# Performance work log

Measured on AMD Instinct MI355X. Metric: run time of the kernel, lower is better.

## Reference

```python
import jax, jax.numpy as jnp
import numpy as np

WIN = 7
K1, K2 = 0.01, 0.03


def _box_filter(x, w):
    """Valid-padding uniform box filter. x: (B, D, H, W); w: (1, 1, k, k)."""
    B, D, H, Wd = x.shape
    k = w.shape[-1]
    y = jax.lax.conv_general_dilated(
        x.reshape(B * D, 1, H, Wd), w, window_strides=(1, 1), padding='VALID',
        dimension_numbers=('NCHW', 'OIHW', 'NCHW'))
    return y.reshape(B, D, H - k + 1, Wd - k + 1)


def setup_inputs() -> dict:
    key = jax.random.key(0)
    kx, ky = jax.random.split(key)
    X = jax.random.uniform(kx, (4, 64, 256, 256), dtype=jnp.float32)
    Y = jax.random.uniform(ky, (4, 64, 256, 256), dtype=jnp.float32)
    w = jnp.ones((1, 1, WIN, WIN), dtype=jnp.float32) / (WIN * WIN)  # buffer self.w
    return {"X": X, "Y": Y, "w": w}


def reference(X, Y, w):
    data_range = 1.0
    C1 = (K1 * data_range) ** 2
    C2 = (K2 * data_range) ** 2
    NP = WIN * WIN
    cov_norm = NP / (NP - 1)

    ux = _box_filter(X, w)
    uy = _box_filter(Y, w)
    uxx = _box_filter(X * X, w)
    uyy = _box_filter(Y * Y, w)
    uxy = _box_filter(X * Y, w)

    vx = cov_norm * (uxx - ux * ux)
    vy = cov_norm * (uyy - uy * uy)
    vxy = cov_norm * (uxy - ux * uy)

    A1 = 2.0 * ux * uy + C1
    A2 = 2.0 * vxy + C2
    B1 = ux * ux + uy * uy + C1
    B2 = vx + vy + C2
    S = (A1 * A2) / (B1 * B2)  # (B, D, H', W')

    # Faithful to torch: ssim_per_slice[:, i] = S_i.mean() (mean over batch AND spatial),
    # then 1 - mean over depth, returned per batch element.
    slice_means = S.mean(axis=(0, 2, 3))  # (D,)
    loss = 1.0 - slice_means.mean()
    return jnp.full((X.shape[0],), loss, dtype=X.dtype)
```

## Files before the change

### kernel.cpp

```cpp
#include <hip/hip_runtime.h>

#define H 256
#define W 256
#define W4 (W / 4)
#define OWID 250
#define NIMG 256
#define BAND 10
#define NBANDS 25
#define NBLK (NBANDS * NIMG)
#define RIN 16
#define WPB 4
#define NBLOCKS (NBLK / WPB)


__device__ __forceinline__ float4 f4zero() { return make_float4(0.f, 0.f, 0.f, 0.f); }

#define CC1 1e-4f
#define CC2 9e-4f
#define KAA (1.f / 2401.f)
#define K2A (2.f / 2401.f)
#define KT1 (1.f / 24.f)
#define KT2 (-1.f / 1176.f)
#define KT3 (1.f / 48.f)
#define KT4 (-1.f / 2352.f)

struct Ctx {
    const float4* Xp;
    const float4* Yp;
    float4 sx, sy, sxy, spp;
    float4 ex[3], ey[3];
    float4 lx, ly;
};

__device__ __forceinline__ void hwin4(const float4 S, float w[4]) {
    const float p1 = S.x;
    const float p2 = p1 + S.y;
    const float p3 = p2 + S.z;
    const float E  = p3 + S.w;
    const float n3 = __shfl_down(p3, 1);
    const float nE = __shfl_down(E, 1);
    const float f1 = __shfl_down(p1, 2);
    const float f2 = __shfl_down(p2, 2);
    w[0] = E + n3;
    w[1] = (E - p1) + nE;
    w[2] = (E - p2) + nE + f1;
    w[3] = (E - p3) + nE + f2;
}

template<int R>
__device__ __forceinline__ void step(Ctx& c, const float m01, const float m23,
                                     float& lsum) {
    const float4 xn = c.ex[R % 3], yn = c.ey[R % 3];
    float4 xo = f4zero(), yo = f4zero();
    if constexpr (R >= 7) { xo = c.lx; yo = c.ly; }

    if constexpr (R + 3 < RIN) {
        c.ex[R % 3] = c.Xp[(R + 3) * W4];
        c.ey[R % 3] = c.Yp[(R + 3) * W4];
    }
    if constexpr (R >= 6 && R <= 14) {
        c.lx = c.Xp[(R - 6) * W4];
        c.ly = c.Yp[(R - 6) * W4];
    }

    c.sx.x += xn.x - xo.x; c.sx.y += xn.y - xo.y;
    c.sx.z += xn.z - xo.z; c.sx.w += xn.w - xo.w;
    c.sy.x += yn.x - yo.x; c.sy.y += yn.y - yo.y;
    c.sy.z += yn.z - yo.z; c.sy.w += yn.w - yo.w;
    c.sxy.x = fmaf(xn.x, yn.x, fmaf(-xo.x, yo.x, c.sxy.x));
    c.sxy.y = fmaf(xn.y, yn.y, fmaf(-xo.y, yo.y, c.sxy.y));
    c.sxy.z = fmaf(xn.z, yn.z, fmaf(-xo.z, yo.z, c.sxy.z));
    c.sxy.w = fmaf(xn.w, yn.w, fmaf(-xo.w, yo.w, c.sxy.w));
    c.spp.x = fmaf(xn.x, xn.x, fmaf(yn.x, yn.x, fmaf(-xo.x, xo.x, fmaf(-yo.x, yo.x, c.spp.x))));
    c.spp.y = fmaf(xn.y, xn.y, fmaf(yn.y, yn.y, fmaf(-xo.y, xo.y, fmaf(-yo.y, yo.y, c.spp.y))));
    c.spp.z = fmaf(xn.z, xn.z, fmaf(yn.z, yn.z, fmaf(-xo.z, xo.z, fmaf(-yo.z, yo.z, c.spp.z))));
    c.spp.w = fmaf(xn.w, xn.w, fmaf(yn.w, yn.w, fmaf(-xo.w, xo.w, fmaf(-yo.w, yo.w, c.spp.w))));

    if constexpr (R >= 6) {
        float wx[4], wy[4], wpp[4], wxy[4];
        hwin4(c.sx,  wx);
        hwin4(c.sy,  wy);
        hwin4(c.spp, wpp);
        hwin4(c.sxy, wxy);
        #pragma unroll
        for (int s = 0; s < 4; ++s) {
            const float P  = wx[s] * wy[s];
            const float Qs = fmaf(wy[s], wy[s], wx[s] * wx[s]);
            const float A1 = fmaf(K2A, P, CC1);
            const float B1 = fmaf(KAA, Qs, CC1);
            const float A2 = fmaf(KT1, wxy[s], fmaf(KT2, P, CC2));
            const float B2 = fmaf(KT3, wpp[s], fmaf(KT4, Qs, CC2));
            const float S  = (A1 * A2) * __builtin_amdgcn_rcpf(B1 * B2);
            lsum = fmaf(S, (s < 2) ? m01 : m23, lsum);
        }
    }
    if constexpr (R + 1 < RIN) step<R + 1>(c, m01, m23, lsum);
}

__global__ __launch_bounds__(256) void ssim_band_kernel(
    const float* __restrict__ X, const float* __restrict__ Y,
    float* __restrict__ partial)
{
    const int lane = threadIdx.x & 63;
    const int wid  = blockIdx.x * WPB + (threadIdx.x >> 6);
    const int img  = wid / NBANDS;
    const int band = wid % NBANDS;
    const int r0 = band * BAND;

    Ctx c;
    c.Xp = (const float4*)X + ((size_t)img * H + r0) * W4 + lane;
    c.Yp = (const float4*)Y + ((size_t)img * H + r0) * W4 + lane;
    c.sx = f4zero(); c.sy = f4zero(); c.sxy = f4zero(); c.spp = f4zero();
    c.ex[0] = c.Xp[0];      c.ey[0] = c.Yp[0];
    c.ex[1] = c.Xp[W4];     c.ey[1] = c.Yp[W4];
    c.ex[2] = c.Xp[2 * W4]; c.ey[2] = c.Yp[2 * W4];
    c.lx = f4zero(); c.ly = f4zero();

    const float m01 = (lane <= 62) ? 1.0f : 0.0f;
    const float m23 = (lane <= 61) ? 1.0f : 0.0f;

    float lsum = 0.0f;
    step<0>(c, m01, m23, lsum);

    #pragma unroll
    for (int off = 32; off > 0; off >>= 1)
        lsum += __shfl_down(lsum, off, 64);
    if (lane == 0) partial[wid] = lsum;
}

__global__ __launch_bounds__(256) void ssim_reduce_kernel(
    const float* __restrict__ partial, float* __restrict__ out)
{
    const int tid = threadIdx.x;
    double acc = 0.0;
    for (int i = tid; i < NBLK; i += 256)
        acc += (double)partial[i];
    #pragma unroll
    for (int off = 32; off > 0; off >>= 1)
        acc += __shfl_down(acc, off, 64);
    __shared__ double wsumd[4];
    if ((tid & 63) == 0) wsumd[tid >> 6] = acc;
    __syncthreads();
    if (tid == 0) {
        double total = wsumd[0] + wsumd[1] + wsumd[2] + wsumd[3];
        float loss = (float)(1.0 - total / 16000000.0);
        out[0] = loss; out[1] = loss; out[2] = loss; out[3] = loss;
    }
}

extern "C" void kernel_launch(void* const* d_in, const int* in_sizes, int n_in,
                              void* d_out, int out_size, void* d_ws, size_t ws_size,
                              hipStream_t stream) {
    const float* X = (const float*)d_in[0];
    const float* Y = (const float*)d_in[1];
    float* out = (float*)d_out;
    float* partial = (float*)d_ws;

    hipLaunchKernelGGL(ssim_band_kernel, dim3(NBLOCKS), dim3(256), 0, stream,
                       X, Y, partial);
    hipLaunchKernelGGL(ssim_reduce_kernel, dim3(1), dim3(256), 0, stream,
                       partial, out);
}
```

Baseline: 158.8 us.

## Stage input rows into an LDS ring via direct global-to-LDS loads

Each wave now streams its band's rows of X and Y into a per-wave LDS ring buffer using global_load_lds with a prefetch distance of two rows. Rows leaving the vertical window are read back from LDS, so the second global reload of old rows goes away. The block size also drops from four waves to two. This trims global traffic and register pressure, but adds LDS use (about 20KB per wave), LDS reads and hand-written waitcnt synchronisation. The shallower prefetch depth may expose more memory latency.

```diff
diff --git a/kernel.cpp b/kernel.cpp
--- a/kernel.cpp
+++ b/kernel.cpp
@@ -9,8 +9,10 @@
 #define NBANDS 25
 #define NBLK (NBANDS * NIMG)
 #define RIN 16
-#define WPB 4
+#define WPB 2
 #define NBLOCKS (NBLK / WPB)
+#define NR 10
+#define PF 2
 
 
 __device__ __forceinline__ float4 f4zero() { return make_float4(0.f, 0.f, 0.f, 0.f); }
@@ -24,13 +26,18 @@
 #define KT3 (1.f / 48.f)
 #define KT4 (-1.f / 2352.f)
 
-struct Ctx {
-    const float4* Xp;
-    const float4* Yp;
-    float4 sx, sy, sxy, spp;
-    float4 ex[3], ey[3];
-    float4 lx, ly;
-};
+__device__ __forceinline__ void stage(const float4* g, float* l) {
+    __builtin_amdgcn_global_load_lds(
+        (const __attribute__((address_space(1))) unsigned int*)g,
+        (__attribute__((address_space(3))) unsigned int*)l,
+        16, 0, 0);
+}
+
+template<int N> __device__ __forceinline__ void wait_vm() {
+    if constexpr (N >= 4)      asm volatile("s_waitcnt vmcnt(4)" ::: "memory");
+    else if constexpr (N == 2) asm volatile("s_waitcnt vmcnt(2)" ::: "memory");
+    else                       asm volatile("s_waitcnt vmcnt(0)" ::: "memory");
+}
 
 __device__ __forceinline__ void hwin4(const float4 S, float w[4]) {
     const float p1 = S.x;
@@ -47,41 +54,54 @@
     w[3] = (E - p3) + nE + f2;
 }
 
+struct K {
+    const float4* Xp;
+    const float4* Yp;
+    float* rx;
+    float* ry;
+    float4 sx, sy, sxy, spp;
+    float m01, m23, lsum;
+    int lane;
+};
+
 template<int R>
-__device__ __forceinline__ void step(Ctx& c, const float m01, const float m23,
-                                     float& lsum) {
-    const float4 xn = c.ex[R % 3], yn = c.ey[R % 3];
+__device__ __forceinline__ void step(K& k) {
+    asm volatile("s_waitcnt lgkmcnt(0)" ::: "memory");
+
+    if constexpr (R + PF < RIN) {
+        stage(k.Xp + (R + PF) * W4, k.rx + ((R + PF) % NR) * W);
+        stage(k.Yp + (R + PF) * W4, k.ry + ((R + PF) % NR) * W);
+    }
+    constexpr int REM = RIN - 1 - R;
+    wait_vm<2 * (REM < PF ? REM : PF)>();
+
+    const float4 xn = *(const float4*)(k.rx + (R % NR) * W + k.lane * 4);
+    const float4 yn = *(const float4*)(k.ry + (R % NR) * W + k.lane * 4);
     float4 xo = f4zero(), yo = f4zero();
-    if constexpr (R >= 7) { xo = c.lx; yo = c.ly; }
-
-    if constexpr (R + 3 < RIN) {
-        c.ex[R % 3] = c.Xp[(R + 3) * W4];
-        c.ey[R % 3] = c.Yp[(R + 3) * W4];
-    }
-    if constexpr (R >= 6 && R <= 14) {
-        c.lx = c.Xp[(R - 6) * W4];
-        c.ly = c.Yp[(R - 6) * W4];
+    if constexpr (R >= 7) {
+        xo = *(const float4*)(k.rx + ((R - 7) % NR) * W + k.lane * 4);
+        yo = *(const float4*)(k.ry + ((R - 7) % NR) * W + k.lane * 4);
     }
 
-    c.sx.x += xn.x - xo.x; c.sx.y += xn.y - xo.y;
-    c.sx.z += xn.z - xo.z; c.sx.w += xn.w - xo.w;
-    c.sy.x += yn.x - yo.x; c.sy.y += yn.y - yo.y;
-    c.sy.z += yn.z - yo.z; c.sy.w += yn.w - yo.w;
-    c.sxy.x = fmaf(xn.x, yn.x, fmaf(-xo.x, yo.x, c.sxy.x));
-    c.sxy.y = fmaf(xn.y, yn.y, fmaf(-xo.y, yo.y, c.sxy.y));
-    c.sxy.z = fmaf(xn.z, yn.z, fmaf(-xo.z, yo.z, c.sxy.z));
-    c.sxy.w = fmaf(xn.w, yn.w, fmaf(-xo.w, yo.w, c.sxy.w));
-    c.spp.x = fmaf(xn.x, xn.x, fmaf(yn.x, yn.x, fmaf(-xo.x, xo.x, fmaf(-yo.x, yo.x, c.spp.x))));
-    c.spp.y = fmaf(xn.y, xn.y, fmaf(yn.y, yn.y, fmaf(-xo.y, xo.y, fmaf(-yo.y, yo.y, c.spp.y))));
-    c.spp.z = fmaf(xn.z, xn.z, fmaf(yn.z, yn.z, fmaf(-xo.z, xo.z, fmaf(-yo.z, yo.z, c.spp.z))));
-    c.spp.w = fmaf(xn.w, xn.w, fmaf(yn.w, yn.w, fmaf(-xo.w, xo.w, fmaf(-yo.w, yo.w, c.spp.w))));
+    k.sx.x += xn.x - xo.x; k.sx.y += xn.y - xo.y;
+    k.sx.z += xn.z - xo.z; k.sx.w += xn.w - xo.w;
+    k.sy.x += yn.x - yo.x; k.sy.y += yn.y - yo.y;
+    k.sy.z += yn.z - yo.z; k.sy.w += yn.w - yo.w;
+    k.sxy.x = fmaf(xn.x, yn.x, fmaf(-xo.x, yo.x, k.sxy.x));
+    k.sxy.y = fmaf(xn.y, yn.y, fmaf(-xo.y, yo.y, k.sxy.y));
+    k.sxy.z = fmaf(xn.z, yn.z, fmaf(-xo.z, yo.z, k.sxy.z));
+    k.sxy.w = fmaf(xn.w, yn.w, fmaf(-xo.w, yo.w, k.sxy.w));
+    k.spp.x = fmaf(xn.x, xn.x, fmaf(yn.x, yn.x, fmaf(-xo.x, xo.x, fmaf(-yo.x, yo.x, k.spp.x))));
+    k.spp.y = fmaf(xn.y, xn.y, fmaf(yn.y, yn.y, fmaf(-xo.y, xo.y, fmaf(-yo.y, yo.y, k.spp.y))));
+    k.spp.z = fmaf(xn.z, xn.z, fmaf(yn.z, yn.z, fmaf(-xo.z, xo.z, fmaf(-yo.z, yo.z, k.spp.z))));
+    k.spp.w = fmaf(xn.w, xn.w, fmaf(yn.w, yn.w, fmaf(-xo.w, xo.w, fmaf(-yo.w, yo.w, k.spp.w))));
 
     if constexpr (R >= 6) {
         float wx[4], wy[4], wpp[4], wxy[4];
-        hwin4(c.sx,  wx);
-        hwin4(c.sy,  wy);
-        hwin4(c.spp, wpp);
-        hwin4(c.sxy, wxy);
+        hwin4(k.sx,  wx);
+        hwin4(k.sy,  wy);
+        hwin4(k.spp, wpp);
+        hwin4(k.sxy, wxy);
         #pragma unroll
         for (int s = 0; s < 4; ++s) {
             const float P  = wx[s] * wy[s];
@@ -91,37 +111,44 @@
             const float A2 = fmaf(KT1, wxy[s], fmaf(KT2, P, CC2));
             const float B2 = fmaf(KT3, wpp[s], fmaf(KT4, Qs, CC2));
             const float S  = (A1 * A2) * __builtin_amdgcn_rcpf(B1 * B2);
-            lsum = fmaf(S, (s < 2) ? m01 : m23, lsum);
+            k.lsum = fmaf(S, (s < 2) ? k.m01 : k.m23, k.lsum);
         }
     }
-    if constexpr (R + 1 < RIN) step<R + 1>(c, m01, m23, lsum);
+    if constexpr (R + 1 < RIN) step<R + 1>(k);
 }
 
-__global__ __launch_bounds__(256) void ssim_band_kernel(
+__global__ __launch_bounds__(128) void ssim_band_kernel(
     const float* __restrict__ X, const float* __restrict__ Y,
     float* __restrict__ partial)
 {
-    const int lane = threadIdx.x & 63;
-    const int wid  = blockIdx.x * WPB + (threadIdx.x >> 6);
-    const int img  = wid / NBANDS;
-    const int band = wid % NBANDS;
+    __shared__ float ring[WPB][2][NR][W];
+
+    const int lane  = threadIdx.x & 63;
+    const int wslot = threadIdx.x >> 6;
+    const int wid   = blockIdx.x * WPB + wslot;
+    const int img   = wid / NBANDS;
+    const int band  = wid % NBANDS;
     const int r0 = band * BAND;
 
-    Ctx c;
-    c.Xp = (const float4*)X + ((size_t)img * H + r0) * W4 + lane;
-    c.Yp = (const float4*)Y + ((size_t)img * H + r0) * W4 + lane;
-    c.sx = f4zero(); c.sy = f4zero(); c.sxy = f4zero(); c.spp = f4zero();
-    c.ex[0] = c.Xp[0];      c.ey[0] = c.Yp[0];
-    c.ex[1] = c.Xp[W4];     c.ey[1] = c.Yp[W4];
-    c.ex[2] = c.Xp[2 * W4]; c.ey[2] = c.Yp[2 * W4];
-    c.lx = f4zero(); c.ly = f4zero();
+    K k;
+    k.Xp = (const float4*)X + ((size_t)img * H + r0) * W4 + lane;
+    k.Yp = (const float4*)Y + ((size_t)img * H + r0) * W4 + lane;
+    k.rx = &ring[wslot][0][0][0];
+    k.ry = &ring[wslot][1][0][0];
+    k.sx = f4zero(); k.sy = f4zero(); k.sxy = f4zero(); k.spp = f4zero();
+    k.lane = lane;
+    k.m01 = (lane <= 62) ? 1.0f : 0.0f;
+    k.m23 = (lane <= 61) ? 1.0f : 0.0f;
+    k.lsum = 0.0f;
 
-    const float m01 = (lane <= 62) ? 1.0f : 0.0f;
-    const float m23 = (lane <= 61) ? 1.0f : 0.0f;
+    stage(k.Xp,            k.rx);
+    stage(k.Yp,            k.ry);
+    stage(k.Xp + W4,       k.rx + W);
+    stage(k.Yp + W4,       k.ry + W);
 
-    float lsum = 0.0f;
-    step<0>(c, m01, m23, lsum);
+    step<0>(k);
 
+    float lsum = k.lsum;
     #pragma unroll
     for (int off = 32; off > 0; off >>= 1)
         lsum += __shfl_down(lsum, off, 64);
@@ -156,7 +183,7 @@
     float* out = (float*)d_out;
     float* partial = (float*)d_ws;
 
-    hipLaunchKernelGGL(ssim_band_kernel, dim3(NBLOCKS), dim3(256), 0, stream,
+    hipLaunchKernelGGL(ssim_band_kernel, dim3(NBLOCKS), dim3(128), 0, stream,
                        X, Y, partial);
     hipLaunchKernelGGL(ssim_reduce_kernel, dim3(1), dim3(256), 0, stream,
                        partial, out);
```

New measurement: 179.3 us. 12.9% more time.

## Process two images per wave and reload evicted rows instead of caching

Applied to the files above, without the earlier changes.

Each wave now handles the same band in two images (img and img+128), interleaving two independent sliding-window chains to raise instruction-level parallelism while halving the wave count to 3200. The lookahead buffers shrink to one row and the rows leaving the window are re-read from memory (expected cache hits) rather than held in registers. The goal is better latency hiding per wave. The cost is fewer waves in flight and more load instructions, which could hurt occupancy-based latency hiding.

```diff
diff --git a/kernel.cpp b/kernel.cpp
--- a/kernel.cpp
+++ b/kernel.cpp
@@ -2,15 +2,14 @@
 
 #define H 256
 #define W 256
-#define W4 (W / 4)
 #define OWID 250
-#define NIMG 256
 #define BAND 10
 #define NBANDS 25
-#define NBLK (NBANDS * NIMG)
+#define NW 3200
+#define WPB 4
+#define NBLOCKS (NW / WPB)
 #define RIN 16
-#define WPB 4
-#define NBLOCKS (NBLK / WPB)
+#define ROWB 1024
 
 
 __device__ __forceinline__ float4 f4zero() { return make_float4(0.f, 0.f, 0.f, 0.f); }
@@ -24,13 +23,27 @@
 #define KT3 (1.f / 48.f)
 #define KT4 (-1.f / 2352.f)
 
-struct Ctx {
-    const float4* Xp;
-    const float4* Yp;
-    float4 sx, sy, sxy, spp;
-    float4 ex[3], ey[3];
-    float4 lx, ly;
-};
+struct M4 { float4 sx, sy, sxy, spp; };
+
+__device__ __forceinline__ float4 ld16(const char* b, int off) {
+    return *(const float4*)(b + off);
+}
+
+__device__ __forceinline__ void slide(M4& m, const float4 xn, const float4 yn,
+                                      const float4 xo, const float4 yo) {
+    m.sx.x += xn.x - xo.x; m.sx.y += xn.y - xo.y;
+    m.sx.z += xn.z - xo.z; m.sx.w += xn.w - xo.w;
+    m.sy.x += yn.x - yo.x; m.sy.y += yn.y - yo.y;
+    m.sy.z += yn.z - yo.z; m.sy.w += yn.w - yo.w;
+    m.sxy.x = fmaf(xn.x, yn.x, fmaf(-xo.x, yo.x, m.sxy.x));
+    m.sxy.y = fmaf(xn.y, yn.y, fmaf(-xo.y, yo.y, m.sxy.y));
+    m.sxy.z = fmaf(xn.z, yn.z, fmaf(-xo.z, yo.z, m.sxy.z));
+    m.sxy.w = fmaf(xn.w, yn.w, fmaf(-xo.w, yo.w, m.sxy.w));
+    m.spp.x = fmaf(xn.x, xn.x, fmaf(yn.x, yn.x, fmaf(-xo.x, xo.x, fmaf(-yo.x, yo.x, m.spp.x))));
+    m.spp.y = fmaf(xn.y, xn.y, fmaf(yn.y, yn.y, fmaf(-xo.y, xo.y, fmaf(-yo.y, yo.y, m.spp.y))));
+    m.spp.z = fmaf(xn.z, xn.z, fmaf(yn.z, yn.z, fmaf(-xo.z, xo.z, fmaf(-yo.z, yo.z, m.spp.z))));
+    m.spp.w = fmaf(xn.w, xn.w, fmaf(yn.w, yn.w, fmaf(-xo.w, xo.w, fmaf(-yo.w, yo.w, m.spp.w))));
+}
 
 __device__ __forceinline__ void hwin4(const float4 S, float w[4]) {
     const float p1 = S.x;
@@ -47,54 +60,63 @@
     w[3] = (E - p3) + nE + f2;
 }
 
+__device__ __forceinline__ void outrow(const M4& m, const float m01,
+                                       const float m23, float& lsum) {
+    float wx[4], wy[4], wpp[4], wxy[4];
+    hwin4(m.sx,  wx);
+    hwin4(m.sy,  wy);
+    hwin4(m.spp, wpp);
+    hwin4(m.sxy, wxy);
+    #pragma unroll
+    for (int s = 0; s < 4; ++s) {
+        const float P  = wx[s] * wy[s];
+        const float Qs = fmaf(wy[s], wy[s], wx[s] * wx[s]);
+        const float A1 = fmaf(K2A, P, CC1);
+        const float B1 = fmaf(KAA, Qs, CC1);
+        const float A2 = fmaf(KT1, wxy[s], fmaf(KT2, P, CC2));
+        const float B2 = fmaf(KT3, wpp[s], fmaf(KT4, Qs, CC2));
+        const float S  = (A1 * A2) * __builtin_amdgcn_rcpf(B1 * B2);
+        lsum = fmaf(S, (s < 2) ? m01 : m23, lsum);
+    }
+}
+
 template<int R>
-__device__ __forceinline__ void step(Ctx& c, const float m01, const float m23,
-                                     float& lsum) {
-    const float4 xn = c.ex[R % 3], yn = c.ey[R % 3];
-    float4 xo = f4zero(), yo = f4zero();
-    if constexpr (R >= 7) { xo = c.lx; yo = c.ly; }
-
-    if constexpr (R + 3 < RIN) {
-        c.ex[R % 3] = c.Xp[(R + 3) * W4];
-        c.ey[R % 3] = c.Yp[(R + 3) * W4];
+__device__ __forceinline__ void step(
+    const char* XA, const char* YA, const char* XB, const char* YB,
+    const int lo, M4& a, M4& b,
+    float4& exA, float4& eyA, float4& exB, float4& eyB,
+    const float m01, const float m23, float& lsum)
+{
+    {
+        const float4 xn = exA, yn = eyA;
+        if constexpr (R + 1 < RIN) {
+            exA = ld16(XA, lo + (R + 1) * ROWB);
+            eyA = ld16(YA, lo + (R + 1) * ROWB);
+        }
+        float4 xo = f4zero(), yo = f4zero();
+        if constexpr (R >= 7) {
+            xo = ld16(XA, lo + (R - 7) * ROWB);
+            yo = ld16(YA, lo + (R - 7) * ROWB);
+        }
+        slide(a, xn, yn, xo, yo);
+        if constexpr (R >= 6) outrow(a, m01, m23, lsum);
     }
-    if constexpr (R >= 6 && R <= 14) {
-        c.lx = c.Xp[(R - 6) * W4];
-        c.ly = c.Yp[(R - 6) * W4];
+    {
+        const float4 xn = exB, yn = eyB;
+        if constexpr (R + 1 < RIN) {
+            exB = ld16(XB, lo + (R + 1) * ROWB);
+            eyB = ld16(YB, lo + (R + 1) * ROWB);
+        }
+        float4 xo = f4zero(), yo = f4zero();
+        if constexpr (R >= 7) {
+            xo = ld16(XB, lo + (R - 7) * ROWB);
+            yo = ld16(YB, lo + (R - 7) * ROWB);
+        }
+        slide(b, xn, yn, xo, yo);
+        if constexpr (R >= 6) outrow(b, m01, m23, lsum);
     }
-
-    c.sx.x += xn.x - xo.x; c.sx.y += xn.y - xo.y;
-    c.sx.z += xn.z - xo.z; c.sx.w += xn.w - xo.w;
-    c.sy.x += yn.x - yo.x; c.sy.y += yn.y - yo.y;
-    c.sy.z += yn.z - yo.z; c.sy.w += yn.w - yo.w;
-    c.sxy.x = fmaf(xn.x, yn.x, fmaf(-xo.x, yo.x, c.sxy.x));
-    c.sxy.y = fmaf(xn.y, yn.y, fmaf(-xo.y, yo.y, c.sxy.y));
-    c.sxy.z = fmaf(xn.z, yn.z, fmaf(-xo.z, yo.z, c.sxy.z));
-    c.sxy.w = fmaf(xn.w, yn.w, fmaf(-xo.w, yo.w, c.sxy.w));
-    c.spp.x = fmaf(xn.x, xn.x, fmaf(yn.x, yn.x, fmaf(-xo.x, xo.x, fmaf(-yo.x, yo.x, c.spp.x))));
-    c.spp.y = fmaf(xn.y, xn.y, fmaf(yn.y, yn.y, fmaf(-xo.y, xo.y, fmaf(-yo.y, yo.y, c.spp.y))));
-    c.spp.z = fmaf(xn.z, xn.z, fmaf(yn.z, yn.z, fmaf(-xo.z, xo.z, fmaf(-yo.z, yo.z, c.spp.z))));
-    c.spp.w = fmaf(xn.w, xn.w, fmaf(yn.w, yn.w, fmaf(-xo.w, xo.w, fmaf(-yo.w, yo.w, c.spp.w))));
-
-    if constexpr (R >= 6) {
-        float wx[4], wy[4], wpp[4], wxy[4];
-        hwin4(c.sx,  wx);
-        hwin4(c.sy,  wy);
-        hwin4(c.spp, wpp);
-        hwin4(c.sxy, wxy);
-        #pragma unroll
-        for (int s = 0; s < 4; ++s) {
-            const float P  = wx[s] * wy[s];
-            const float Qs = fmaf(wy[s], wy[s], wx[s] * wx[s]);
-            const float A1 = fmaf(K2A, P, CC1);
-            const float B1 = fmaf(KAA, Qs, CC1);
-            const float A2 = fmaf(KT1, wxy[s], fmaf(KT2, P, CC2));
-            const float B2 = fmaf(KT3, wpp[s], fmaf(KT4, Qs, CC2));
-            const float S  = (A1 * A2) * __builtin_amdgcn_rcpf(B1 * B2);
-            lsum = fmaf(S, (s < 2) ? m01 : m23, lsum);
-        }
-    }
-    if constexpr (R + 1 < RIN) step<R + 1>(c, m01, m23, lsum);
+    if constexpr (R + 1 < RIN)
+        step<R + 1>(XA, YA, XB, YB, lo, a, b, exA, eyA, exB, eyB, m01, m23, lsum);
 }
 
 __global__ __launch_bounds__(256) void ssim_band_kernel(
@@ -103,24 +125,30 @@
 {
     const int lane = threadIdx.x & 63;
     const int wid  = blockIdx.x * WPB + (threadIdx.x >> 6);
-    const int img  = wid / NBANDS;
+    const int imgA = wid / NBANDS;
     const int band = wid % NBANDS;
     const int r0 = band * BAND;
 
-    Ctx c;
-    c.Xp = (const float4*)X + ((size_t)img * H + r0) * W4 + lane;
-    c.Yp = (const float4*)Y + ((size_t)img * H + r0) * W4 + lane;
-    c.sx = f4zero(); c.sy = f4zero(); c.sxy = f4zero(); c.spp = f4zero();
-    c.ex[0] = c.Xp[0];      c.ey[0] = c.Yp[0];
-    c.ex[1] = c.Xp[W4];     c.ey[1] = c.Yp[W4];
-    c.ex[2] = c.Xp[2 * W4]; c.ey[2] = c.Yp[2 * W4];
-    c.lx = f4zero(); c.ly = f4zero();
+    const size_t baseA = ((size_t)imgA * H + r0) * ROWB;
+    const size_t dB    = (size_t)128 * H * ROWB;
+    const char* XA = (const char*)X + baseA;
+    const char* YA = (const char*)Y + baseA;
+    const char* XB = XA + dB;
+    const char* YB = YA + dB;
+    const int lo = lane * 16;
+
+    M4 a, b;
+    a.sx = f4zero(); a.sy = f4zero(); a.sxy = f4zero(); a.spp = f4zero();
+    b.sx = f4zero(); b.sy = f4zero(); b.sxy = f4zero(); b.spp = f4zero();
+
+    float4 exA = ld16(XA, lo), eyA = ld16(YA, lo);
+    float4 exB = ld16(XB, lo), eyB = ld16(YB, lo);
 
     const float m01 = (lane <= 62) ? 1.0f : 0.0f;
     const float m23 = (lane <= 61) ? 1.0f : 0.0f;
 
     float lsum = 0.0f;
-    step<0>(c, m01, m23, lsum);
+    step<0>(XA, YA, XB, YB, lo, a, b, exA, eyA, exB, eyB, m01, m23, lsum);
 
     #pragma unroll
     for (int off = 32; off > 0; off >>= 1)
@@ -133,7 +161,7 @@
 {
     const int tid = threadIdx.x;
     double acc = 0.0;
-    for (int i = tid; i < NBLK; i += 256)
+    for (int i = tid; i < NW; i += 256)
         acc += (double)partial[i];
     #pragma unroll
     for (int off = 32; off > 0; off >>= 1)
```

Result: slower. 162.6 us (+2.4%).
